# Kernel optimization log

Measured on AMD Instinct MI355X. Metric: run time of the kernel, lower is better.

Reference implementation:

```python
import jax, jax.numpy as jnp
import numpy as np

HIDDEN = 512
NUM_HEADS = 8
HEAD_DIM = HIDDEN // NUM_HEADS


def setup_inputs() -> dict:
    key = jax.random.key(0)
    k1, k2 = jax.random.split(key)
    x = jax.random.normal(k1, (2, 2048, HIDDEN), dtype=jnp.float32)
    # torch Linear(h, 3h, bias=False): weight shape [3h, h], y = x @ W.T
    W_qkv = jax.random.normal(k2, (3 * HIDDEN, HIDDEN), dtype=jnp.float32) * (HIDDEN ** -0.5)
    return {"x": x, "W_qkv": W_qkv}


def reference(x, W_qkv):
    B, S, h = x.shape
    H, d = NUM_HEADS, HEAD_DIM
    temperature = (1.0 / d) ** 0.5  # sqrt(1/head_dim)
    qkv = x @ W_qkv.T  # [B, S, 3h]
    # Original chunks 3h into H pieces of size 3d (per-head interleaved QKV),
    # stacks on dim=1 -> [B, H, S, 3d], then splits into Q, K, V.
    qkv = qkv.reshape(B, S, H, 3 * d).transpose(0, 2, 1, 3)  # [B, H, S, 3d]
    q, k, v = jnp.split(qkv, 3, axis=-1)  # each [B, H, S, d]
    scores = jnp.einsum("bhqd,bhkd->bhqk", q * temperature, k)  # [B, H, S, S]
    # dropout is inference no-op; mask branch in original is a dead assignment
    w = jax.nn.softmax(scores, axis=-1)
    out = jnp.einsum("bhqk,bhkd->bhqd", w, v)  # [B, H, S, d]
    # torch.cat over heads on last dim == transpose back + merge heads
    return out.transpose(0, 2, 1, 3).reshape(B, S, h)
```

## Files before the change

### kernel.cpp

```cpp
#include <hip/hip_runtime.h>
#include <stdint.h>

#define HD 512
#define NH 8
#define DH 64
#define SEQ 2048
#define BATCH 2
#define M_TOTAL (BATCH*SEQ)
#define N_QKV (3*HD)
#define K_DIM HD

typedef short bf16x8 __attribute__((ext_vector_type(8)));
typedef float f32x4 __attribute__((ext_vector_type(4)));
typedef uint32_t u32x2 __attribute__((ext_vector_type(2)));
typedef uint32_t u32x4 __attribute__((ext_vector_type(4)));

#define QSCALE 0.18033688011112042f

__device__ __forceinline__ uint16_t f2bf(float f) {
  union { float f; uint32_t u; } v; v.f = f;
  uint32_t u = v.u;
  return (uint16_t)((u + 0x7FFFu + ((u >> 16) & 1u)) >> 16);
}

__device__ __forceinline__ void gload_lds16(const void* g, void* l) {
  __builtin_amdgcn_global_load_lds(
      (const __attribute__((address_space(1))) void*)g,
      (__attribute__((address_space(3))) void*)l,
      16, 0, 0);
}

__global__ void convert_all(const float* __restrict__ x, const float* __restrict__ W,
                            uint16_t* __restrict__ xb, uint16_t* __restrict__ Wb) {
  const int nx4 = M_TOTAL * K_DIM / 4;
  const int nw4 = N_QKV * K_DIM / 4;
  int i = blockIdx.x * 256 + threadIdx.x;
  const float* src; uint16_t* dst; int j;
  if (i < nx4) { src = x; dst = xb; j = i; }
  else { j = i - nx4; if (j >= nw4) return; src = W; dst = Wb; }
  float4 v = reinterpret_cast<const float4*>(src)[j];
  ushort4 o;
  o.x = f2bf(v.x); o.y = f2bf(v.y); o.z = f2bf(v.z); o.w = f2bf(v.w);
  reinterpret_cast<ushort4*>(dst)[j] = o;
}

#define BM 64
#define BN 128
#define BK 64
#define NKT (K_DIM / BK)

__global__ __launch_bounds__(256)
void qkv_gemm(const uint16_t* __restrict__ A,
              const uint16_t* __restrict__ Bw,
              uint16_t* __restrict__ C,
              uint16_t* __restrict__ Vt) {
  __shared__ __align__(16) uint16_t As[2][BM * BK];
  __shared__ __align__(16) uint16_t Bs[2][BN * BK];

  const int t = threadIdx.x;
  const int lane = t & 63;
  const int w = t >> 6;
  const int l15 = lane & 15, l4 = lane >> 4;

  const int nbx = gridDim.x;
  const int nwg = nbx * gridDim.y;
  const int cpx = nwg >> 3;
  int id = blockIdx.y * nbx + blockIdx.x;
  int wid = (id & 7) * cpx + (id >> 3);
  const int m0 = (wid / nbx) * BM;
  const int n0 = (wid % nbx) * BN;

  f32x4 acc[4][2] = {};

  auto stage = [&](int kt, int buf) {
#pragma unroll
    for (int i = 0; i < 2; ++i) {
      int idx = t + 256 * i;
      int row = idx >> 3, slot = idx & 7;
      int src = slot ^ (row & 7);
      gload_lds16(A + (size_t)(m0 + row) * K_DIM + kt * BK + src * 8,
                  (char*)As[buf] + idx * 16);
    }
#pragma unroll
    for (int i = 0; i < 4; ++i) {
      int idx = t + 256 * i;
      int row = idx >> 3, slot = idx & 7;
      int src = slot ^ (row & 7);
      gload_lds16(Bw + (size_t)(n0 + row) * K_DIM + kt * BK + src * 8,
                  (char*)Bs[buf] + idx * 16);
    }
  };

  stage(0, 0);
  for (int kt = 0; kt < NKT; ++kt) {
    __syncthreads();
    if (kt + 1 < NKT) stage(kt + 1, (kt + 1) & 1);
    const char* Ab = (const char*)As[kt & 1];
    const char* Bb = (const char*)Bs[kt & 1];
#pragma unroll
    for (int kk = 0; kk < 2; ++kk) {
      bf16x8 af[4], bf[2];
#pragma unroll
      for (int i = 0; i < 4; ++i) {
        int rowa = i * 16 + l15;
        int sa = (kk * 4 + l4) ^ (rowa & 7);
        af[i] = *reinterpret_cast<const bf16x8*>(Ab + rowa * 128 + sa * 16);
      }
#pragma unroll
      for (int j = 0; j < 2; ++j) {
        int rowb = w * 32 + j * 16 + l15;
        int sb = (kk * 4 + l4) ^ (rowb & 7);
        bf[j] = *reinterpret_cast<const bf16x8*>(Bb + rowb * 128 + sb * 16);
      }
#pragma unroll
      for (int i = 0; i < 4; ++i)
#pragma unroll
        for (int j = 0; j < 2; ++j)
          acc[i][j] = __builtin_amdgcn_mfma_f32_16x16x32_bf16(af[i], bf[j], acc[i][j], 0, 0, 0);
    }
  }

  const int colw = n0 + w * 32;
  const int cmod = colw % 192;
  const bool isv = (cmod >= 128);
  __syncthreads();

  if (isv) {
    char* tb = (char*)As + w * 4096;
#pragma unroll
    for (int i = 0; i < 4; ++i)
#pragma unroll
      for (int j = 0; j < 2; ++j) {
        uint32_t lo, hi;
        asm("v_cvt_pk_bf16_f32 %0, %1, %2" : "=v"(lo) : "v"(acc[i][j][0]), "v"(acc[i][j][1]));
        asm("v_cvt_pk_bf16_f32 %0, %1, %2" : "=v"(hi) : "v"(acc[i][j][2]), "v"(acc[i][j][3]));
        int dloc = j * 16 + l15;
        int slot_s = i * 2 + (l4 >> 1);
        int byteoff = dloc * 128 + ((slot_s ^ (dloc & 7)) * 16) + (l4 & 1) * 8;
        u32x2 pk; pk.x = lo; pk.y = hi;
        *reinterpret_cast<u32x2*>(tb + byteoff) = pk;
      }
    int h = colw / 192;
    int d0 = cmod - 128;
    int b = m0 >> 11;
    int sbase = m0 & (SEQ - 1);
    uint16_t* vbase = Vt + ((size_t)(b * NH + h) * DH + d0) * SEQ + sbase + (lane & 7) * 8;
#pragma unroll
    for (int p = 0; p < 4; ++p) {
      int dl = p * 8 + (lane >> 3);
      u32x4 rv = *reinterpret_cast<const u32x4*>(
          tb + dl * 128 + (((lane & 7) ^ (dl & 7)) * 16));
      *reinterpret_cast<u32x4*>(vbase + (size_t)dl * SEQ) = rv;
    }
  } else {
    float sc = ((cmod >> 6) == 0) ? QSCALE : 1.0f;
#pragma unroll
    for (int i = 0; i < 4; ++i) {
      int row = m0 + i * 16 + l4 * 4;
#pragma unroll
      for (int j = 0; j < 2; ++j) {
        int col = colw + j * 16 + l15;
#pragma unroll
        for (int jj = 0; jj < 4; ++jj)
          C[(size_t)(row + jj) * N_QKV + col] = f2bf(acc[i][j][jj] * sc);
      }
    }
  }
}

#define KVB 32
#define NT2 (SEQ / KVB)

__global__ __launch_bounds__(256, 8)
void attn(const uint16_t* __restrict__ qkv, const uint16_t* __restrict__ VtG,
          float* __restrict__ Po,
          float2* __restrict__ Pml) {
  __shared__ __align__(16) uint16_t Kt[2][KVB * 64];
  __shared__ __align__(16) uint16_t Vt[2][DH * KVB];
  __shared__ __align__(16) uint16_t Pl[4][16 * KVB];

  const int t = threadIdx.x;
  const int lane = t & 63;
  const int w = t >> 6;
  const int l15 = lane & 15, l4 = lane >> 4;
  const int bh = blockIdx.x;
  const int b = bh >> 3, h = bh & 7;
  const int qw = blockIdx.y * 64 + w * 16;
  const int half = blockIdx.z;
  const int tph = NT2 / gridDim.z;
  const int t0 = half * tph;

  bf16x8 qf[2];
  {
    const uint16_t* qp = qkv + (size_t)(b * SEQ + qw + l15) * N_QKV + h * 192;
#pragma unroll
    for (int kk = 0; kk < 2; ++kk)
      qf[kk] = *reinterpret_cast<const bf16x8*>(qp + kk * 32 + l4 * 8);
  }

  const uint16_t* kgbase = qkv + (size_t)b * SEQ * N_QKV + h * 192 + 64;
  const uint16_t* vgbase = VtG + (size_t)bh * DH * SEQ;

  auto stage = [&](int ti, int buf) {
    int s0 = ti * KVB;
    {
      int row = t >> 3, slot = t & 7;
      int src = slot ^ (row & 7);
      gload_lds16(kgbase + (size_t)(s0 + row) * N_QKV + src * 8,
                  (char*)Kt[buf] + t * 16);
    }
    {
      int d = t >> 2, slot = t & 3;
      int src = slot ^ (d & 3);
      gload_lds16(vgbase + (size_t)d * SEQ + s0 + src * 8,
                  (char*)Vt[buf] + t * 16);
    }
  };

  f32x4 ot[4] = {};
  float mrow = -1e30f, lrow = 0.0f;

  stage(t0, 0);
  for (int rel = 0; rel < tph; ++rel) {
    __syncthreads();
    if (rel + 1 < tph) stage(t0 + rel + 1, (rel + 1) & 1);
    const char* Kb = (const char*)Kt[rel & 1];
    const char* Vb = (const char*)Vt[rel & 1];

    f32x4 s[2] = {};
    __builtin_amdgcn_s_setprio(1);
#pragma unroll
    for (int c = 0; c < 2; ++c) {
#pragma unroll
      for (int kk = 0; kk < 2; ++kk) {
        int row = c * 16 + l15;
        int sl = (kk * 4 + l4) ^ (row & 7);
        bf16x8 kf = *reinterpret_cast<const bf16x8*>(Kb + row * 128 + sl * 16);
        s[c] = __builtin_amdgcn_mfma_f32_16x16x32_bf16(kf, qf[kk], s[c], 0, 0, 0);
      }
    }
    __builtin_amdgcn_s_setprio(0);

    float vmax = s[0][0];
#pragma unroll
    for (int c = 0; c < 2; ++c)
#pragma unroll
      for (int jj = 0; jj < 4; ++jj) vmax = fmaxf(vmax, s[c][jj]);
    vmax = fmaxf(vmax, __shfl_xor(vmax, 16, 64));
    vmax = fmaxf(vmax, __shfl_xor(vmax, 32, 64));

    if (!__all(vmax - mrow <= 11.0f)) {
      float mn = fmaxf(mrow, vmax);
      float sc;
      float darg = mrow - mn;
      asm("v_exp_f32 %0, %1" : "=v"(sc) : "v"(darg));
      mrow = mn;
#pragma unroll
      for (int f = 0; f < 4; ++f)
#pragma unroll
        for (int jj = 0; jj < 4; ++jj) ot[f][jj] *= sc;
      lrow *= sc;
    }

    float p[8];
#pragma unroll
    for (int c = 0; c < 2; ++c)
#pragma unroll
      for (int jj = 0; jj < 4; ++jj) {
        float arg = s[c][jj] - mrow;
        float e;
        asm("v_exp_f32 %0, %1" : "=v"(e) : "v"(arg));
        p[c * 4 + jj] = e;
      }
    float tsum = ((p[0] + p[1]) + (p[2] + p[3])) + ((p[4] + p[5]) + (p[6] + p[7]));
    tsum += __shfl_xor(tsum, 16, 64);
    tsum += __shfl_xor(tsum, 32, 64);
    lrow += tsum;

#pragma unroll
    for (int c = 0; c < 2; ++c) {
      uint32_t lo, hi;
      asm("v_cvt_pk_bf16_f32 %0, %1, %2" : "=v"(lo) : "v"(p[c * 4 + 0]), "v"(p[c * 4 + 1]));
      asm("v_cvt_pk_bf16_f32 %0, %1, %2" : "=v"(hi) : "v"(p[c * 4 + 2]), "v"(p[c * 4 + 3]));
      int slot = 2 * c + (l4 >> 1);
      int byteoff = l15 * 64 + ((slot ^ (l15 & 3)) * 16) + (l4 & 1) * 8;
      u32x2 pk; pk.x = lo; pk.y = hi;
      *reinterpret_cast<u32x2*>((char*)Pl[w] + byteoff) = pk;
    }

    int sp = l4 ^ (l15 & 3);
    bf16x8 pa = *reinterpret_cast<const bf16x8*>((const char*)Pl[w] + l15 * 64 + sp * 16);
    __builtin_amdgcn_s_setprio(1);
#pragma unroll
    for (int f = 0; f < 4; ++f) {
      int d = f * 16 + l15;
      int sv = l4 ^ (d & 3);
      bf16x8 vf = *reinterpret_cast<const bf16x8*>(Vb + d * 64 + sv * 16);
      ot[f] = __builtin_amdgcn_mfma_f32_16x16x32_bf16(vf, pa, ot[f], 0, 0, 0);
    }
    __builtin_amdgcn_s_setprio(0);
  }

  float* pob = Po + ((size_t)(half * 16 + bh) * SEQ) * DH + (size_t)(qw + l15) * DH;
#pragma unroll
  for (int f = 0; f < 4; ++f)
    *reinterpret_cast<f32x4*>(pob + f * 16 + l4 * 4) = ot[f];
  if (lane < 16) {
    float2 ml; ml.x = mrow; ml.y = lrow;
    Pml[(size_t)(half * 16 + bh) * SEQ + qw + lane] = ml;
  }
}

__global__ __launch_bounds__(256)
void attn_combine(const float* __restrict__ Po, const float2* __restrict__ Pml,
                  float* __restrict__ out, int nsplit) {
  int idx = blockIdx.x * 256 + threadIdx.x;
  int d4 = idx & 15;
  int q = (idx >> 4) & (SEQ - 1);
  int bh = idx >> 15;
  int b = bh >> 3, h = bh & 7;

  float m = -1e30f;
  for (int s = 0; s < nsplit; ++s)
    m = fmaxf(m, Pml[(size_t)(s * 16 + bh) * SEQ + q].x);
  float den = 0.0f;
  f32x4 acc = {};
  for (int s = 0; s < nsplit; ++s) {
    float2 ml = Pml[(size_t)(s * 16 + bh) * SEQ + q];
    float a = exp2f(ml.x - m);
    den += ml.y * a;
    f32x4 ov = *reinterpret_cast<const f32x4*>(
        Po + ((size_t)(s * 16 + bh) * SEQ + q) * DH + d4 * 4);
#pragma unroll
    for (int i = 0; i < 4; ++i) acc[i] += ov[i] * a;
  }
  float rden = 1.0f / den;
  f32x4 res;
#pragma unroll
  for (int i = 0; i < 4; ++i) res[i] = acc[i] * rden;
  *reinterpret_cast<f32x4*>(out + ((size_t)(b * SEQ + q) * HD) + h * 64 + d4 * 4) = res;
}

extern "C" void kernel_launch(void* const* d_in, const int* in_sizes, int n_in,
                              void* d_out, int out_size, void* d_ws, size_t ws_size,
                              hipStream_t stream) {
  const float* x = (const float*)d_in[0];
  const float* Wq = (const float*)d_in[1];
  float* out = (float*)d_out;

  uint16_t* xb = (uint16_t*)d_ws;
  uint16_t* Wb = xb + (size_t)M_TOTAL * K_DIM;
  uint16_t* qkv = Wb + (size_t)N_QKV * K_DIM;
  uint16_t* vtg = qkv + (size_t)M_TOTAL * N_QKV;
  float* Po = (float*)(vtg + (size_t)16 * DH * SEQ);
  float2* Pml = (float2*)(Po + (size_t)4 * 16 * SEQ * DH);
  size_t base = (size_t)((char*)Po - (char*)d_ws);
  size_t per_split = (size_t)16 * SEQ * DH * 4 + (size_t)16 * SEQ * 8;
  int nsplit = 1;
  if (ws_size >= base + 4 * per_split) nsplit = 4;
  else if (ws_size >= base + 2 * per_split) nsplit = 2;

  convert_all<<<(M_TOTAL * K_DIM / 4 + N_QKV * K_DIM / 4 + 255) / 256, 256, 0, stream>>>(
      x, Wq, xb, Wb);

  dim3 g1(N_QKV / BN, M_TOTAL / BM);
  qkv_gemm<<<g1, 256, 0, stream>>>(xb, Wb, qkv, vtg);

  dim3 g2(BATCH * NH, SEQ / 64, nsplit);
  attn<<<g2, 256, 0, stream>>>(qkv, vtg, Po, Pml);

  attn_combine<<<(16 * SEQ * 16) / 256, 256, 0, stream>>>(Po, Pml, out, nsplit);
}
```

Before: 121.4 us.

## Load V fragments directly from global into registers instead of LDS staging

The attention kernel stops staging V tiles through shared memory. Each wave now reads its V MFMA operands straight from global memory into registers at the top of each KV iteration, which removes the V LDS buffers and their reads. The P scratch buffer switches from an XOR swizzle to a padded row stride (80 bytes) to avoid bank conflicts, and the occupancy hint drops from 8 to 5 blocks. The cost is that global-load latency is now exposed inside the loop with no double buffering, and every wave fetches V separately instead of the block sharing one staged copy.

```diff
diff --git a/kernel.cpp b/kernel.cpp
--- a/kernel.cpp
+++ b/kernel.cpp
@@ -170,14 +170,14 @@
 
 #define KVB 32
 #define NT2 (SEQ / KVB)
-
-__global__ __launch_bounds__(256, 8)
+#define PLS 80
+
+__global__ __launch_bounds__(256, 5)
 void attn(const uint16_t* __restrict__ qkv, const uint16_t* __restrict__ VtG,
           float* __restrict__ Po,
           float2* __restrict__ Pml) {
   __shared__ __align__(16) uint16_t Kt[2][KVB * 64];
-  __shared__ __align__(16) uint16_t Vt[2][DH * KVB];
-  __shared__ __align__(16) uint16_t Pl[4][16 * KVB];
+  __shared__ __align__(16) uint8_t Pl[4][16 * PLS];
 
   const int t = threadIdx.x;
   const int lane = t & 63;
@@ -201,31 +201,30 @@
   const uint16_t* kgbase = qkv + (size_t)b * SEQ * N_QKV + h * 192 + 64;
   const uint16_t* vgbase = VtG + (size_t)bh * DH * SEQ;
 
-  auto stage = [&](int ti, int buf) {
+  auto stageK = [&](int ti, int buf) {
     int s0 = ti * KVB;
-    {
-      int row = t >> 3, slot = t & 7;
-      int src = slot ^ (row & 7);
-      gload_lds16(kgbase + (size_t)(s0 + row) * N_QKV + src * 8,
-                  (char*)Kt[buf] + t * 16);
-    }
-    {
-      int d = t >> 2, slot = t & 3;
-      int src = slot ^ (d & 3);
-      gload_lds16(vgbase + (size_t)d * SEQ + s0 + src * 8,
-                  (char*)Vt[buf] + t * 16);
-    }
+    int row = t >> 3, slot = t & 7;
+    int src = slot ^ (row & 7);
+    gload_lds16(kgbase + (size_t)(s0 + row) * N_QKV + src * 8,
+                (char*)Kt[buf] + t * 16);
   };
 
   f32x4 ot[4] = {};
   float mrow = -1e30f, lrow = 0.0f;
 
-  stage(t0, 0);
+  stageK(t0, 0);
   for (int rel = 0; rel < tph; ++rel) {
     __syncthreads();
-    if (rel + 1 < tph) stage(t0 + rel + 1, (rel + 1) & 1);
+    int s0 = (t0 + rel) * KVB;
+
+    bf16x8 vf[4];
+#pragma unroll
+    for (int f = 0; f < 4; ++f)
+      vf[f] = *reinterpret_cast<const bf16x8*>(
+          vgbase + (size_t)(f * 16 + l15) * SEQ + s0 + l4 * 8);
+
+    if (rel + 1 < tph) stageK(t0 + rel + 1, (rel + 1) & 1);
     const char* Kb = (const char*)Kt[rel & 1];
-    const char* Vb = (const char*)Vt[rel & 1];
 
     f32x4 s[2] = {};
     __builtin_amdgcn_s_setprio(1);
@@ -283,21 +282,16 @@
       asm("v_cvt_pk_bf16_f32 %0, %1, %2" : "=v"(lo) : "v"(p[c * 4 + 0]), "v"(p[c * 4 + 1]));
       asm("v_cvt_pk_bf16_f32 %0, %1, %2" : "=v"(hi) : "v"(p[c * 4 + 2]), "v"(p[c * 4 + 3]));
       int slot = 2 * c + (l4 >> 1);
-      int byteoff = l15 * 64 + ((slot ^ (l15 & 3)) * 16) + (l4 & 1) * 8;
+      int byteoff = l15 * PLS + slot * 16 + (l4 & 1) * 8;
       u32x2 pk; pk.x = lo; pk.y = hi;
       *reinterpret_cast<u32x2*>((char*)Pl[w] + byteoff) = pk;
     }
 
-    int sp = l4 ^ (l15 & 3);
-    bf16x8 pa = *reinterpret_cast<const bf16x8*>((const char*)Pl[w] + l15 * 64 + sp * 16);
+    bf16x8 pa = *reinterpret_cast<const bf16x8*>((const char*)Pl[w] + l15 * PLS + l4 * 16);
     __builtin_amdgcn_s_setprio(1);
 #pragma unroll
-    for (int f = 0; f < 4; ++f) {
-      int d = f * 16 + l15;
-      int sv = l4 ^ (d & 3);
-      bf16x8 vf = *reinterpret_cast<const bf16x8*>(Vb + d * 64 + sv * 16);
-      ot[f] = __builtin_amdgcn_mfma_f32_16x16x32_bf16(vf, pa, ot[f], 0, 0, 0);
-    }
+    for (int f = 0; f < 4; ++f)
+      ot[f] = __builtin_amdgcn_mfma_f32_16x16x32_bf16(vf[f], pa, ot[f], 0, 0, 0);
     __builtin_amdgcn_s_setprio(0);
   }
 
```

Result: slower. 158.0 us (+30.1%).
